# Optimization experiments

Measured on AMD Instinct MI355X. Metric: run time of the kernel, lower is better.

The kernel has to match this reference:

```python
import jax, jax.numpy as jnp
import numpy as np

DIM = 384
HEADS = 8
ADLA = 343
HWD = 14
N = HWD ** 3
B = 8
HEAD_DIM = DIM // HEADS
SCALE = HEAD_DIM ** -0.5
POOL = 7  # ceil(343**(1/3)); 14 is evenly divisible by 7


def _lin_mat(in_size, out_size):
    # PyTorch trilinear interpolation (align_corners=False), one axis -> (out,in) matrix
    scale = in_size / out_size
    x = (np.arange(out_size) + 0.5) * scale - 0.5
    x = np.clip(x, 0.0, in_size - 1)
    x0 = np.floor(x).astype(np.int64)
    x1 = np.minimum(x0 + 1, in_size - 1)
    w = (x - x0).astype(np.float32)
    M = np.zeros((out_size, in_size), np.float32)
    M[np.arange(out_size), x0] += 1.0 - w
    M[np.arange(out_size), x1] += w
    return jnp.asarray(M)


def _interp3(t, out_hwd):
    # t: (..., a, b, c) -> (..., H, W, D) trilinear, align_corners=False
    Ma = _lin_mat(t.shape[-3], out_hwd[0])
    Mb = _lin_mat(t.shape[-2], out_hwd[1])
    Mc = _lin_mat(t.shape[-1], out_hwd[2])
    return jnp.einsum('...abc,xa,yb,zc->...xyz', t, Ma, Mb, Mc)


def setup_inputs() -> dict:
    key = jax.random.key(0)
    ks = jax.random.split(key, 16)
    std = 0.02
    return {
        'x': jax.random.normal(ks[0], (B, N, DIM), jnp.float32),
        'Wq': jax.random.normal(ks[1], (DIM, DIM), jnp.float32) * std,
        'Wkv': jax.random.normal(ks[2], (DIM, 2 * DIM), jnp.float32) * std,
        'Wproj': jax.random.normal(ks[3], (DIM, DIM), jnp.float32) * std,
        'bproj': jnp.zeros((DIM,), jnp.float32),
        'dwc_w': jax.random.normal(ks[4], (DIM, 1, 3, 3, 3), jnp.float32) * std,
        'dwc_b': jnp.zeros((DIM,), jnp.float32),
        'an_bias': jax.random.normal(ks[5], (HEADS, ADLA, 7, 7, 7), jnp.float32) * std,
        'na_bias': jax.random.normal(ks[6], (HEADS, ADLA, 7, 7, 7), jnp.float32) * std,
        'ah_bias': jax.random.normal(ks[7], (1, HEADS, ADLA, HWD, 1, 1), jnp.float32) * std,
        'aw_bias': jax.random.normal(ks[8], (1, HEADS, ADLA, 1, HWD, 1), jnp.float32) * std,
        'ad_bias': jax.random.normal(ks[9], (1, HEADS, ADLA, 1, 1, HWD), jnp.float32) * std,
        'ha_bias': jax.random.normal(ks[10], (1, HEADS, HWD, 1, 1, ADLA), jnp.float32) * std,
        'wa_bias': jax.random.normal(ks[11], (1, HEADS, 1, HWD, 1, ADLA), jnp.float32) * std,
        'da_bias': jax.random.normal(ks[12], (1, HEADS, 1, 1, HWD, ADLA), jnp.float32) * std,
        'H': HWD, 'W': HWD, 'D': HWD,
    }


def reference(x, Wq, Wkv, Wproj, bproj, dwc_w, dwc_b, an_bias, na_bias,
              ah_bias, aw_bias, ad_bias, ha_bias, wa_bias, da_bias, H, W, D):
    b, n, c = x.shape
    h, hd = HEADS, c // HEADS
    q = x @ Wq                       # (b, n, c)
    kv = x @ Wkv                     # (b, n, 2c)  (sr_ratio == 1)
    k, v = kv[..., :c], kv[..., c:]
    # AdaptiveAvgPool3d 14->7: even 2x2x2 block mean; spatial flatten order matches torch
    adla = q.reshape(b, POOL, H // POOL, POOL, W // POOL, POOL, D // POOL, c)
    adla = adla.mean(axis=(2, 4, 6)).reshape(b, ADLA, c)   # (b, A, c)
    qh = q.reshape(b, n, h, hd).transpose(0, 2, 1, 3)       # (b,h,n,hd)
    kh = k.reshape(b, n, h, hd).transpose(0, 2, 1, 3)
    vh = v.reshape(b, n, h, hd).transpose(0, 2, 1, 3)
    ath = adla.reshape(b, ADLA, h, hd).transpose(0, 2, 1, 3)  # (b,h,A,hd)
    # stage 1: anchor -> tokens
    pb1 = _interp3(an_bias, (H, W, D)).reshape(1, h, ADLA, n)
    pb2 = (ah_bias + aw_bias + ad_bias).reshape(1, h, ADLA, n)
    logits1 = jnp.einsum('bhad,bhnd->bhan', ath * SCALE, kh) + pb1 + pb2
    adla_v = jnp.einsum('bhan,bhnd->bhad', jax.nn.softmax(logits1, axis=-1), vh)
    # stage 2: tokens -> anchor
    ab1 = _interp3(na_bias, (H, W, D)).reshape(1, h, ADLA, n).transpose(0, 1, 3, 2)
    ab2 = (ha_bias + wa_bias + da_bias).reshape(1, h, n, ADLA)
    logits2 = jnp.einsum('bhnd,bhad->bhna', qh * SCALE, ath) + ab1 + ab2
    out = jnp.einsum('bhna,bhad->bhnd', jax.nn.softmax(logits2, axis=-1), adla_v)
    out = out.transpose(0, 2, 1, 3).reshape(b, n, c)
    # depthwise Conv3d on v volume, fused into residual
    vvol = v.reshape(b, H, W, D, c).transpose(0, 4, 1, 2, 3)  # (b,c,H,W,D)
    dwc = jax.lax.conv_general_dilated(
        vvol, dwc_w, (1, 1, 1), 'SAME',
        dimension_numbers=('NCDHW', 'OIDHW', 'NCDHW'), feature_group_count=c)
    dwc = dwc + dwc_b[None, :, None, None, None]
    out = out + dwc.transpose(0, 2, 3, 4, 1).reshape(b, n, c)
    return out @ Wproj + bproj
```

## Files before the change

### kernel.cpp

```cpp
#include <hip/hip_runtime.h>
#include <hip/hip_bf16.h>
#include <cstdint>

typedef __bf16 bf16;
typedef __attribute__((ext_vector_type(8))) __bf16 bf16x8;
typedef __attribute__((ext_vector_type(4))) __bf16 bf16x4;
typedef __attribute__((ext_vector_type(2))) __bf16 bf16x2;
typedef __attribute__((ext_vector_type(4))) float f32x4;

constexpr int DIM = 384;
constexpr int HEAD_DIM = 48;
constexpr int ADLA_N = 343;
constexpr int NTOK = 2744;
constexpr int BATCH = 8;
constexpr int MTOT = BATCH * NTOK;
constexpr float SCALE = 0.14433756729740643f;
constexpr int B1W = 2816;
constexpr int B2W = 384;
constexpr int ADV_W = 352;
constexpr int SEG = 6;

__global__ void transpose_weights(const float* __restrict__ Wq,
                                  const float* __restrict__ Wkv,
                                  const float* __restrict__ Wproj,
                                  bf16* __restrict__ WTall,
                                  bf16* __restrict__ WprojT) {
  int idx = blockIdx.x * 256 + threadIdx.x;
  const int total1 = 1152 * 384;
  if (idx < total1) {
    int j = idx / 384, k = idx % 384;
    WTall[idx] = (bf16)((j < 384) ? Wq[k * 384 + j] : Wkv[k * 768 + (j - 384)]);
  } else {
    int i2 = idx - total1;
    if (i2 < 384 * 384) {
      int j = i2 / 384, k = i2 % 384;
      WprojT[i2] = (bf16)Wproj[k * 384 + j];
    }
  }
}

__device__ __forceinline__ void lin_w(int i, int& i0, int& i1, float& w) {
  float f = 0.5f * (float)i - 0.25f;
  f = fminf(fmaxf(f, 0.0f), 6.0f);
  i0 = (int)f;
  w = f - (float)i0;
  i1 = (i0 + 1 < 7) ? i0 + 1 : 6;
}

__device__ __forceinline__ float interp3(const float* __restrict__ p, int x, int y, int z) {
  int x0, x1, y0, y1, z0, z1; float wx, wy, wz;
  lin_w(x, x0, x1, wx); lin_w(y, y0, y1, wy); lin_w(z, z0, z1, wz);
  float c000 = p[x0*49 + y0*7 + z0], c001 = p[x0*49 + y0*7 + z1];
  float c010 = p[x0*49 + y1*7 + z0], c011 = p[x0*49 + y1*7 + z1];
  float c100 = p[x1*49 + y0*7 + z0], c101 = p[x1*49 + y0*7 + z1];
  float c110 = p[x1*49 + y1*7 + z0], c111 = p[x1*49 + y1*7 + z1];
  float c00 = c000 + wz * (c001 - c000), c01 = c010 + wz * (c011 - c010);
  float c10 = c100 + wz * (c101 - c100), c11 = c110 + wz * (c111 - c110);
  float c0 = c00 + wy * (c01 - c00), c1 = c10 + wy * (c11 - c10);
  return c0 + wx * (c1 - c0);
}

__global__ void bias1_kernel(const float* __restrict__ an, const float* __restrict__ ah,
                             const float* __restrict__ aw, const float* __restrict__ ad,
                             bf16* __restrict__ out) {
  int h = blockIdx.x / ADLA_N, a = blockIdx.x % ADLA_N;
  const float* anp = an + ((size_t)h * ADLA_N + a) * 343;
  const float* ahp = ah + ((size_t)h * ADLA_N + a) * 14;
  const float* awp = aw + ((size_t)h * ADLA_N + a) * 14;
  const float* adp = ad + ((size_t)h * ADLA_N + a) * 14;
  bf16* op = out + ((size_t)h * ADLA_N + a) * B1W;
  for (int n = threadIdx.x; n < B1W; n += 256) {
    if (n < NTOK) {
      int x = n / 196, y = (n / 14) % 14, z = n % 14;
      float v = interp3(anp, x, y, z) + ahp[x] + awp[y] + adp[z];
      op[n] = (bf16)v;
    } else {
      op[n] = (bf16)0.f;
    }
  }
}

__global__ __launch_bounds__(256)
void bias2_kernel(const float* __restrict__ na, const float* __restrict__ ha,
                  const float* __restrict__ wa, const float* __restrict__ da,
                  bf16* __restrict__ out) {
  __shared__ bf16 t[64 * 66];
  const int tid = threadIdx.x;
  const int wv = tid >> 6, lane = tid & 63;
  const int n0 = blockIdx.x * 64, a0 = blockIdx.y * 64;
  const int h = blockIdx.z;
  const int nc = min(n0 + lane, NTOK - 1);
  const int x = nc / 196, y = (nc / 14) % 14, z = nc % 14;
  int x0, x1, y0, y1, z0, z1; float wx, wy, wz;
  lin_w(x, x0, x1, wx); lin_w(y, y0, y1, wy); lin_w(z, z0, z1, wz);
  const int o[8] = { x0*49 + y0*7 + z0, x0*49 + y0*7 + z1,
                     x0*49 + y1*7 + z0, x0*49 + y1*7 + z1,
                     x1*49 + y0*7 + z0, x1*49 + y0*7 + z1,
                     x1*49 + y1*7 + z0, x1*49 + y1*7 + z1 };
  const float wgt[8] = { (1.f-wx)*(1.f-wy)*(1.f-wz), (1.f-wx)*(1.f-wy)*wz,
                         (1.f-wx)*wy*(1.f-wz),       (1.f-wx)*wy*wz,
                         wx*(1.f-wy)*(1.f-wz),       wx*(1.f-wy)*wz,
                         wx*wy*(1.f-wz),             wx*wy*wz };
#pragma unroll
  for (int j = 0; j < 16; j++) {
    const int al = wv * 16 + j;
    const int a = a0 + al;
    float s = 0.f;
    if (a < ADLA_N) {
      const float* p = na + ((size_t)h * ADLA_N + a) * 343;
#pragma unroll
      for (int k = 0; k < 8; k++) s += p[o[k]] * wgt[k];
      s += ha[((size_t)h * 14 + x) * ADLA_N + a]
         + wa[((size_t)h * 14 + y) * ADLA_N + a]
         + da[((size_t)h * 14 + z) * ADLA_N + a];
    }
    t[lane * 66 + al] = (bf16)s;
  }
  __syncthreads();
#pragma unroll
  for (int j = 0; j < 16; j++) {
    const int nr = wv * 16 + j;
    if (n0 + nr < NTOK)
      out[((size_t)h * NTOK + n0 + nr) * B2W + a0 + lane] = t[nr * 66 + lane];
  }
}

template <int MODE, typename AT, typename OT>
__global__ __launch_bounds__(256)
void gemm128(const AT* __restrict__ A, const bf16* __restrict__ BT, int M,
             OT* __restrict__ O0, bf16* __restrict__ O1, bf16* __restrict__ O2,
             const float* __restrict__ bias) {
  __shared__ __align__(16) bf16 As[128 * 40];
  __shared__ __align__(16) bf16 Bs[128 * 40];
  const int tid = threadIdx.x;
  const int wv = tid >> 6, lane = tid & 63;
  const int m0 = blockIdx.x * 128, n0 = blockIdx.y * 128;
  const int wr = wv >> 1, wc = wv & 1;
  f32x4 zero4 = {0.f, 0.f, 0.f, 0.f};
  f32x4 acc[4][4];
#pragma unroll
  for (int i = 0; i < 4; i++)
#pragma unroll
    for (int j = 0; j < 4; j++) acc[i][j] = zero4;

  for (int k0 = 0; k0 < 384; k0 += 32) {
    __syncthreads();
#pragma unroll
    for (int i = 0; i < 2; i++) {
      int flat = i * 256 + tid;
      int row = flat >> 2, cg = flat & 3;
      int gr = m0 + row; if (gr >= M) gr = M - 1;
      bf16x8 av;
      if constexpr (sizeof(AT) == 4) {
        const float4* s4 = (const float4*)(A + (size_t)gr * 384 + k0 + cg * 8);
        float4 a = s4[0], b = s4[1];
        av[0]=(bf16)a.x; av[1]=(bf16)a.y; av[2]=(bf16)a.z; av[3]=(bf16)a.w;
        av[4]=(bf16)b.x; av[5]=(bf16)b.y; av[6]=(bf16)b.z; av[7]=(bf16)b.w;
      } else {
        av = *(const bf16x8*)(A + (size_t)gr * 384 + k0 + cg * 8);
      }
      *(bf16x8*)(As + row * 40 + cg * 8) = av;
      int nr = n0 + row;
      *(bf16x8*)(Bs + row * 40 + cg * 8) = *(const bf16x8*)(BT + (size_t)nr * 384 + k0 + cg * 8);
    }
    __syncthreads();
    bf16x8 af[4], bfr[4];
#pragma unroll
    for (int t = 0; t < 4; t++) {
      af[t]  = *(const bf16x8*)(As + (wr * 64 + t * 16 + (lane & 15)) * 40 + (lane >> 4) * 8);
      bfr[t] = *(const bf16x8*)(Bs + (wc * 64 + t * 16 + (lane & 15)) * 40 + (lane >> 4) * 8);
    }
#pragma unroll
    for (int rt = 0; rt < 4; rt++)
#pragma unroll
      for (int ct = 0; ct < 4; ct++)
        acc[rt][ct] = __builtin_amdgcn_mfma_f32_16x16x32_bf16(af[rt], bfr[ct], acc[rt][ct], 0, 0, 0);
  }
  const int quad = lane >> 4, colL = lane & 15;
#pragma unroll
  for (int rt = 0; rt < 4; rt++) {
#pragma unroll
    for (int ct = 0; ct < 4; ct++) {
      int gcol = n0 + wc * 64 + ct * 16 + colL;
#pragma unroll
      for (int r = 0; r < 4; r++) {
        int grow = m0 + wr * 64 + rt * 16 + quad * 4 + r;
        if (grow < M) {
          float v = acc[rt][ct][r];
          if (MODE == 1) {
            v += bias[gcol];
            O0[(size_t)grow * 384 + gcol] = (OT)v;
          } else {
            bf16* dst; int c;
            if (gcol < 384)      { dst = (bf16*)O0; c = gcol; }
            else if (gcol < 768) { dst = O1; c = gcol - 384; }
            else                 { dst = O2; c = gcol - 768; }
            dst[(size_t)grow * 384 + c] = (bf16)v;
          }
        }
      }
    }
  }
}

__global__ void transpose_v(const bf16* __restrict__ v, bf16* __restrict__ vT) {
  __shared__ bf16 t[64][65];
  int n0 = blockIdx.x * 64, c0 = blockIdx.y * 64, b = blockIdx.z;
  int tid = threadIdx.x;
  int cl = tid & 63, rs = tid >> 6;
  for (int j = 0; j < 16; j++) {
    int r = rs * 16 + j;
    int n = n0 + r;
    if (n < NTOK) t[cl][r] = v[((size_t)b * NTOK + n) * DIM + c0 + cl];
  }
  __syncthreads();
  int nl = tid & 63, cs = tid >> 6;
  int n = n0 + nl;
  if (n < NTOK)
    for (int j = 0; j < 16; j++) {
      int cc = cs * 16 + j;
      vT[((size_t)b * DIM + c0 + cc) * NTOK + n] = t[cc][nl];
    }
}

__global__ void pool_kernel(const bf16* __restrict__ q, bf16* __restrict__ adla) {
  int idx = blockIdx.x * 256 + threadIdx.x;
  if (idx >= BATCH * ADLA_N * DIM) return;
  int c = idx % DIM;
  int a = (idx / DIM) % ADLA_N;
  int b = idx / (DIM * ADLA_N);
  int a0 = a / 49, a1 = (a / 7) % 7, a2 = a % 7;
  float s = 0.f;
#pragma unroll
  for (int i = 0; i < 2; i++)
#pragma unroll
    for (int j = 0; j < 2; j++)
#pragma unroll
      for (int k = 0; k < 2; k++) {
        int n = (a0 * 2 + i) * 196 + (a1 * 2 + j) * 14 + (a2 * 2 + k);
        s += (float)q[((size_t)b * NTOK + n) * DIM + c];
      }
  adla[idx] = (bf16)(s * 0.125f);
}

template <int MODE>
__global__ __launch_bounds__(256)
void attn_kernel(const bf16* __restrict__ Amat, const bf16* __restrict__ Kmat,
                 const bf16* __restrict__ Vt, const bf16* __restrict__ Bias,
                 bf16* __restrict__ Out, float* __restrict__ OutP,
                 float* __restrict__ RsP,
                 int AR, int NC, int biasW,
                 size_t vtB, size_t vtH, int vtS) {
  __shared__ __align__(16) bf16 aT[64 * 64];
  __shared__ __align__(16) bf16 kT[128 * 64];
  __shared__ __align__(16) bf16 vTs[48 * 128];
  __shared__ __align__(16) bf16 pT[64 * 128];
  const int tid = threadIdx.x;
  const int wv = tid >> 6, lane = tid & 63;
  const int bh = blockIdx.y;
  const int bI = bh >> 3, h = bh & 7;
  const int r0 = blockIdx.x * 64;
  const int quad = lane >> 4, colL = lane & 15;

#pragma unroll
  for (int i = 0; i < 2; i++) {
    int flat = i * 256 + tid;
    int row = flat >> 3, cg = flat & 7;
    int r = r0 + row; if (r >= AR) r = AR - 1;
    bf16x8 val;
#pragma unroll
    for (int e = 0; e < 8; e++) val[e] = (bf16)0.f;
    if (cg < 6) val = *(const bf16x8*)(Amat + ((size_t)bI * AR + r) * DIM + h * HEAD_DIM + cg * 8);
    *(bf16x8*)(aT + row * 64 + ((cg ^ (row & 7)) << 3)) = val;
  }

  f32x4 zero4 = {0.f, 0.f, 0.f, 0.f};
  f32x4 acc[3] = {zero4, zero4, zero4};
  float rowsum = 0.f;
  const int nCh = (NC + 127) >> 7;
  const int ch0 = blockIdx.z * 4;
  const int ch1 = min(nCh, ch0 + 4);
  const int rowL = wv * 16 + colL;
  const bf16* biasRow = Bias + ((size_t)h * AR + r0 + rowL) * biasW + quad * 4;

  for (int ch = ch0; ch < ch1; ch++) {
    const int c0 = ch << 7;
    __syncthreads();
#pragma unroll
    for (int i = 0; i < 4; i++) {
      int flat = i * 256 + tid;
      int row = flat >> 3, cg = flat & 7;
      int kg = (cg < 6) ? cg : 0;
      int gr = c0 + row; if (gr >= NC) gr = NC - 1;
      *(bf16x8*)(kT + row * 64 + ((cg ^ (row & 7)) << 3)) =
          *(const bf16x8*)(Kmat + ((size_t)bI * NC + gr) * DIM + h * HEAD_DIM + kg * 8);
    }
#pragma unroll
    for (int i = 0; i < 3; i++) {
      int flat = i * 256 + tid;
      int d = flat >> 4, cg = flat & 15;
      int cc = c0 + cg * 8; if (cc > vtS - 8) cc = vtS - 8;
      *(bf16x8*)(vTs + d * 128 + ((cg ^ (d & 15)) << 3)) =
          *(const bf16x8*)(Vt + (size_t)bI * vtB + (size_t)h * vtH + (size_t)d * vtS + cc);
    }
    __syncthreads();

    bf16x4 bv[8];
#pragma unroll
    for (int ct = 0; ct < 8; ct++)
      bv[ct] = *(const bf16x4*)(biasRow + c0 + ct * 16);

    bf16x8 af0 = *(const bf16x8*)(aT + rowL * 64 + ((quad ^ (rowL & 7)) << 3));
    bf16x8 af1 = *(const bf16x8*)(aT + rowL * 64 + (((4 | quad) ^ (rowL & 7)) << 3));
    f32x4 sacc[8];
#pragma unroll
    for (int ct = 0; ct < 8; ct++) sacc[ct] = zero4;
#pragma unroll
    for (int ct = 0; ct < 8; ct++) {
      int krow = ct * 16 + colL;
      bf16x8 b0 = *(const bf16x8*)(kT + krow * 64 + ((quad ^ (krow & 7)) << 3));
      bf16x8 b1 = *(const bf16x8*)(kT + krow * 64 + (((4 | quad) ^ (krow & 7)) << 3));
      sacc[ct] = __builtin_amdgcn_mfma_f32_16x16x32_bf16(b0, af0, sacc[ct], 0, 0, 0);
      sacc[ct] = __builtin_amdgcn_mfma_f32_16x16x32_bf16(b1, af1, sacc[ct], 0, 0, 0);
    }
#pragma unroll
    for (int ct = 0; ct < 8; ct++) {
      int cbase = c0 + ct * 16 + quad * 4;
      bf16x4 pw;
#pragma unroll
      for (int j = 0; j < 4; j++) {
        float s = sacc[ct][j] * SCALE + (float)bv[ct][j];
        s = fminf(fmaxf(s, -60.f), 60.f);
        float p = ((cbase + j) < NC) ? __expf(s) : 0.f;
        rowsum += p;
        pw[j] = (bf16)p;
      }
      int cg = ct * 2 + (quad >> 1);
      *(bf16x4*)(pT + rowL * 128 + ((cg ^ (rowL & 15)) << 3) + (quad & 1) * 4) = pw;
    }
#pragma unroll
    for (int ks = 0; ks < 4; ks++) {
      bf16x8 pf = *(const bf16x8*)(pT + rowL * 128 + (((ks * 4 + quad) ^ (rowL & 15)) << 3));
#pragma unroll
      for (int dt = 0; dt < 3; dt++) {
        const int vrow = dt * 16 + colL;
        bf16x8 vf = *(const bf16x8*)(vTs + vrow * 128 + (((ks * 4 + quad) ^ (vrow & 15)) << 3));
        acc[dt] = __builtin_amdgcn_mfma_f32_16x16x32_bf16(pf, vf, acc[dt], 0, 0, 0);
      }
    }
  }

  rowsum += __shfl_xor(rowsum, 16, 64);
  rowsum += __shfl_xor(rowsum, 32, 64);

  if (MODE == 0) {
    const int seg = blockIdx.z;
#pragma unroll
    for (int dt = 0; dt < 3; dt++)
#pragma unroll
      for (int r = 0; r < 4; r++) {
        int a = r0 + wv * 16 + quad * 4 + r;
        size_t rowD = ((size_t)seg * 64 + bh) * 48 + dt * 16 + colL;
        if (a < AR)
          OutP[rowD * ADV_W + a] = acc[dt][r];
        else if (a < ADV_W)
          OutP[rowD * ADV_W + a] = 0.f;
      }
    if (quad == 0) {
      int a = r0 + rowL;
      if (a < AR)
        RsP[((size_t)seg * 64 + bh) * ADV_W + a] = rowsum;
    }
  } else {
    float inv[4];
#pragma unroll
    for (int r = 0; r < 4; r++) inv[r] = 1.f / __shfl(rowsum, quad * 4 + r, 64);
#pragma unroll
    for (int dt = 0; dt < 3; dt++)
#pragma unroll
      for (int r = 0; r < 4; r++) {
        int n = r0 + wv * 16 + quad * 4 + r;
        if (n < AR)
          Out[((size_t)bI * AR + n) * DIM + h * HEAD_DIM + dt * 16 + colL] = (bf16)(acc[dt][r] * inv[r]);
      }
  }
}

__global__ void attn1_reduce(const float* __restrict__ advP, const float* __restrict__ rsP,
                             bf16* __restrict__ advT) {
  int idx = blockIdx.x * 256 + threadIdx.x;
  if (idx >= 64 * 48 * ADV_W) return;
  int a = idx % ADV_W;
  int d = (idx / ADV_W) % 48;
  int bh = idx / (ADV_W * 48);
  if (a >= ADLA_N) { advT[idx] = (bf16)0.f; return; }
  float s = 0.f, rs = 0.f;
#pragma unroll
  for (int g = 0; g < SEG; g++) {
    s  += advP[(((size_t)g * 64 + bh) * 48 + d) * ADV_W + a];
    rs += rsP[((size_t)g * 64 + bh) * ADV_W + a];
  }
  advT[((size_t)bh * 48 + d) * ADV_W + a] = (bf16)(s / rs);
}

__global__ __launch_bounds__(256)
void dwc_kernel(const bf16* __restrict__ v, const float* __restrict__ w,
                const float* __restrict__ bias, bf16* __restrict__ io) {
  __shared__ float wts[128 * 27];
  const int tid = threadIdx.x;
  const int cg = blockIdx.y;
  const int b  = blockIdx.z;
  for (int i = tid; i < 128 * 27; i += 256)
    wts[i] = w[(size_t)cg * 128 * 27 + i];
  __syncthreads();

  const int wv = tid >> 6, lane = tid & 63;
  const int xy = blockIdx.x * 4 + wv;
  const int x = xy / 14, y = xy % 14;
  const int c0 = lane * 2;
  const int cglob = cg * 128 + c0;
  const bf16* vb_ = v + (size_t)b * NTOK * DIM + cglob;
  bf16* iob = io + (size_t)b * NTOK * DIM + cglob + (size_t)(x * 196 + y * 14) * DIM;

  float2 acc[14];
#pragma unroll
  for (int z = 0; z < 14; z++) acc[z] = make_float2(0.f, 0.f);

#pragma unroll
  for (int dx = -1; dx <= 1; dx++) {
    int X = x + dx; if ((unsigned)X >= 14u) continue;
#pragma unroll
    for (int dy = -1; dy <= 1; dy++) {
      int Y = y + dy; if ((unsigned)Y >= 14u) continue;
      const bf16* colp = vb_ + (size_t)(X * 196 + Y * 14) * DIM;
      float2 col[14];
#pragma unroll
      for (int z = 0; z < 14; z++) {
        bf16x2 u = *(const bf16x2*)(colp + (size_t)z * DIM);
        col[z] = make_float2((float)u[0], (float)u[1]);
      }
      const int tb = (dx + 1) * 9 + (dy + 1) * 3;
      const float w0a = wts[c0 * 27 + tb],     w0b = wts[(c0 + 1) * 27 + tb];
      const float w1a = wts[c0 * 27 + tb + 1], w1b = wts[(c0 + 1) * 27 + tb + 1];
      const float w2a = wts[c0 * 27 + tb + 2], w2b = wts[(c0 + 1) * 27 + tb + 2];
#pragma unroll
      for (int z = 0; z < 14; z++) {
        float2 s = acc[z];
        if (z > 0)  { s.x += col[z - 1].x * w0a; s.y += col[z - 1].y * w0b; }
        s.x += col[z].x * w1a; s.y += col[z].y * w1b;
        if (z < 13) { s.x += col[z + 1].x * w2a; s.y += col[z + 1].y * w2b; }
        acc[z] = s;
      }
    }
  }

  const float bsa = bias[cglob], bsb = bias[cglob + 1];
#pragma unroll
  for (int z = 0; z < 14; z++) {
    bf16x2 u = *(const bf16x2*)(iob + (size_t)z * DIM);
    bf16x2 o;
    o[0] = (bf16)((float)u[0] + acc[z].x + bsa);
    o[1] = (bf16)((float)u[1] + acc[z].y + bsb);
    *(bf16x2*)(iob + (size_t)z * DIM) = o;
  }
}

extern "C" void kernel_launch(void* const* d_in, const int* in_sizes, int n_in,
                              void* d_out, int out_size, void* d_ws, size_t ws_size,
                              hipStream_t stream) {
  const float* x     = (const float*)d_in[0];
  const float* Wq    = (const float*)d_in[1];
  const float* Wkv   = (const float*)d_in[2];
  const float* Wproj = (const float*)d_in[3];
  const float* bproj = (const float*)d_in[4];
  const float* dwcw  = (const float*)d_in[5];
  const float* dwcb  = (const float*)d_in[6];
  const float* an    = (const float*)d_in[7];
  const float* na    = (const float*)d_in[8];
  const float* ahb   = (const float*)d_in[9];
  const float* awb   = (const float*)d_in[10];
  const float* adb   = (const float*)d_in[11];
  const float* hab   = (const float*)d_in[12];
  const float* wab   = (const float*)d_in[13];
  const float* dab   = (const float*)d_in[14];
  float* out = (float*)d_out;

  uint8_t* ws = (uint8_t*)d_ws;
  size_t off = 0;
  auto carveB = [&](size_t bytes) -> void* {
    void* p = ws + off;
    off += ((bytes + 255) & ~(size_t)255);
    return p;
  };
  auto carve = [&](size_t elems) -> bf16* { return (bf16*)carveB(elems * 2); };
  bf16*  wtall  = carve((size_t)1152 * 384);
  bf16*  wprojT = carve((size_t)384 * 384);
  bf16*  qb     = carve((size_t)MTOT * 384 + 128);
  bf16*  kb     = carve((size_t)MTOT * 384 + 128);
  bf16*  vb     = carve((size_t)MTOT * 384 + 128);
  bf16*  vTb    = carve((size_t)MTOT * 384 + 128);
  bf16*  adla   = carve((size_t)BATCH * ADLA_N * 384 + 128);
  bf16*  advT   = carve((size_t)64 * 48 * ADV_W + 128);
  bf16*  bias1  = carve((size_t)8 * ADLA_N * B1W);
  float* advP   = (float*)carveB((size_t)SEG * 64 * 48 * ADV_W * 4);
  float* rsP    = (float*)carveB((size_t)SEG * 64 * ADV_W * 4);
  bf16*  bias2  = kb;
  bf16*  aout   = vTb;

  transpose_weights<<<dim3((1152 * 384 + 384 * 384 + 255) / 256), 256, 0, stream>>>(
      Wq, Wkv, Wproj, wtall, wprojT);
  bias1_kernel<<<dim3(8 * ADLA_N), 256, 0, stream>>>(an, ahb, awb, adb, bias1);
  gemm128<0, float, bf16><<<dim3(172, 9), 256, 0, stream>>>(
      x, wtall, MTOT, qb, kb, vb, nullptr);
  transpose_v<<<dim3(43, 6, 8), 256, 0, stream>>>(vb, vTb);
  pool_kernel<<<dim3((BATCH * ADLA_N * DIM + 255) / 256), 256, 0, stream>>>(qb, adla);
  attn_kernel<0><<<dim3(6, 64, SEG), 256, 0, stream>>>(
      adla, kb, vTb, bias1, nullptr, advP, rsP,
      ADLA_N, NTOK, B1W, (size_t)384 * NTOK, (size_t)48 * NTOK, NTOK);
  attn1_reduce<<<dim3((64 * 48 * ADV_W + 255) / 256), 256, 0, stream>>>(advP, rsP, advT);
  bias2_kernel<<<dim3(43, 6, 8), 256, 0, stream>>>(na, hab, wab, dab, bias2);
  attn_kernel<1><<<dim3(43, 64, 1), 256, 0, stream>>>(
      qb, adla, advT, bias2, aout, nullptr, nullptr,
      NTOK, ADLA_N, B2W, (size_t)8 * 48 * ADV_W, (size_t)48 * ADV_W, ADV_W);
  dwc_kernel<<<dim3(49, 3, 8), 256, 0, stream>>>(vb, dwcw, dwcb, aout);
  gemm128<1, bf16, float><<<dim3(172, 3), 256, 0, stream>>>(
      aout, wprojT, MTOT, out, nullptr, nullptr, bproj);
}
```

Before: 462.2 us.

## Prefetch next K/V tile into registers and load A fragments directly

Register-prefetches the next chunk's K and V tiles while the current chunk's MFMAs run, then writes them to shared memory after a barrier, overlapping global latency with compute. It also drops the shared-memory staging of the A (query/anchor) tile and loads each lane's A fragments straight from global memory. The bias row index is now clamped for out-of-range rows. The cost is higher register pressure from the held prefetch registers, plus an extra barrier per chunk.

```diff
diff --git a/kernel.cpp b/kernel.cpp
--- a/kernel.cpp
+++ b/kernel.cpp
@@ -251,7 +251,6 @@
                  float* __restrict__ RsP,
                  int AR, int NC, int biasW,
                  size_t vtB, size_t vtH, int vtS) {
-  __shared__ __align__(16) bf16 aT[64 * 64];
   __shared__ __align__(16) bf16 kT[128 * 64];
   __shared__ __align__(16) bf16 vTs[48 * 128];
   __shared__ __align__(16) bf16 pT[64 * 128];
@@ -261,18 +260,15 @@
   const int bI = bh >> 3, h = bh & 7;
   const int r0 = blockIdx.x * 64;
   const int quad = lane >> 4, colL = lane & 15;
-
-#pragma unroll
-  for (int i = 0; i < 2; i++) {
-    int flat = i * 256 + tid;
-    int row = flat >> 3, cg = flat & 7;
-    int r = r0 + row; if (r >= AR) r = AR - 1;
-    bf16x8 val;
-#pragma unroll
-    for (int e = 0; e < 8; e++) val[e] = (bf16)0.f;
-    if (cg < 6) val = *(const bf16x8*)(Amat + ((size_t)bI * AR + r) * DIM + h * HEAD_DIM + cg * 8);
-    *(bf16x8*)(aT + row * 64 + ((cg ^ (row & 7)) << 3)) = val;
-  }
+  const int rowL = wv * 16 + colL;
+
+  int ar = r0 + rowL; if (ar >= AR) ar = AR - 1;
+  const bf16* aRow = Amat + ((size_t)bI * AR + ar) * DIM + h * HEAD_DIM;
+  bf16x8 af0 = *(const bf16x8*)(aRow + quad * 8);
+  bf16x8 af1;
+#pragma unroll
+  for (int e = 0; e < 8; e++) af1[e] = (bf16)0.f;
+  if (quad < 2) af1 = *(const bf16x8*)(aRow + 32 + quad * 8);
 
   f32x4 zero4 = {0.f, 0.f, 0.f, 0.f};
   f32x4 acc[3] = {zero4, zero4, zero4};
@@ -280,38 +276,57 @@
   const int nCh = (NC + 127) >> 7;
   const int ch0 = blockIdx.z * 4;
   const int ch1 = min(nCh, ch0 + 4);
-  const int rowL = wv * 16 + colL;
-  const bf16* biasRow = Bias + ((size_t)h * AR + r0 + rowL) * biasW + quad * 4;
-
-  for (int ch = ch0; ch < ch1; ch++) {
+  int br = r0 + rowL; if (br >= AR) br = AR - 1;
+  const bf16* biasRow = Bias + ((size_t)h * AR + br) * biasW + quad * 4;
+
+  bf16x8 kreg[4], vreg[3];
+  auto load_tile = [&](int ch) {
     const int c0 = ch << 7;
-    __syncthreads();
 #pragma unroll
     for (int i = 0; i < 4; i++) {
       int flat = i * 256 + tid;
       int row = flat >> 3, cg = flat & 7;
       int kg = (cg < 6) ? cg : 0;
       int gr = c0 + row; if (gr >= NC) gr = NC - 1;
-      *(bf16x8*)(kT + row * 64 + ((cg ^ (row & 7)) << 3)) =
-          *(const bf16x8*)(Kmat + ((size_t)bI * NC + gr) * DIM + h * HEAD_DIM + kg * 8);
+      kreg[i] = *(const bf16x8*)(Kmat + ((size_t)bI * NC + gr) * DIM + h * HEAD_DIM + kg * 8);
     }
 #pragma unroll
     for (int i = 0; i < 3; i++) {
       int flat = i * 256 + tid;
       int d = flat >> 4, cg = flat & 15;
       int cc = c0 + cg * 8; if (cc > vtS - 8) cc = vtS - 8;
-      *(bf16x8*)(vTs + d * 128 + ((cg ^ (d & 15)) << 3)) =
-          *(const bf16x8*)(Vt + (size_t)bI * vtB + (size_t)h * vtH + (size_t)d * vtS + cc);
-    }
-    __syncthreads();
+      vreg[i] = *(const bf16x8*)(Vt + (size_t)bI * vtB + (size_t)h * vtH + (size_t)d * vtS + cc);
+    }
+  };
+  auto write_tile = [&]() {
+#pragma unroll
+    for (int i = 0; i < 4; i++) {
+      int flat = i * 256 + tid;
+      int row = flat >> 3, cg = flat & 7;
+      *(bf16x8*)(kT + row * 64 + ((cg ^ (row & 7)) << 3)) = kreg[i];
+    }
+#pragma unroll
+    for (int i = 0; i < 3; i++) {
+      int flat = i * 256 + tid;
+      int d = flat >> 4, cg = flat & 15;
+      *(bf16x8*)(vTs + d * 128 + ((cg ^ (d & 15)) << 3)) = vreg[i];
+    }
+  };
+
+  load_tile(ch0);
+  write_tile();
+  __syncthreads();
+
+  for (int ch = ch0; ch < ch1; ch++) {
+    const int c0 = ch << 7;
+    const bool hasNext = (ch + 1 < ch1);
+    if (hasNext) load_tile(ch + 1);
 
     bf16x4 bv[8];
 #pragma unroll
     for (int ct = 0; ct < 8; ct++)
       bv[ct] = *(const bf16x4*)(biasRow + c0 + ct * 16);
 
-    bf16x8 af0 = *(const bf16x8*)(aT + rowL * 64 + ((quad ^ (rowL & 7)) << 3));
-    bf16x8 af1 = *(const bf16x8*)(aT + rowL * 64 + (((4 | quad) ^ (rowL & 7)) << 3));
     f32x4 sacc[8];
 #pragma unroll
     for (int ct = 0; ct < 8; ct++) sacc[ct] = zero4;
@@ -347,6 +362,11 @@
         bf16x8 vf = *(const bf16x8*)(vTs + vrow * 128 + (((ks * 4 + quad) ^ (vrow & 15)) << 3));
         acc[dt] = __builtin_amdgcn_mfma_f32_16x16x32_bf16(pf, vf, acc[dt], 0, 0, 0);
       }
+    }
+    __syncthreads();
+    if (hasNext) {
+      write_tile();
+      __syncthreads();
     }
   }
 
```

Result: faster. 433.5 us (-6.2%).
